# Kernel optimization log

Hardware: AMD Instinct MI355X
Metric: run time of the kernel (lower is better)

Reference implementation:

```python
import jax, jax.numpy as jnp
import numpy as np

EPS = 1e-7

def segment_softmax(logits, seg, num_segments):
    # Numerically-stable softmax over edges grouped by destination node,
    # applied independently per feature column (logits: [E, D]).
    m = jax.ops.segment_max(logits, seg, num_segments=num_segments)  # [N, D]
    e = jnp.exp(logits - m[seg])                                     # [E, D]
    s = jax.ops.segment_sum(e, seg, num_segments=num_segments)       # [N, D]
    return e / s[seg]

def setup_inputs() -> dict:
    key = jax.random.key(0)
    N, E, D_IN, D_OUT = 50000, 800000, 64, 64
    ks = jax.random.split(key, 4)
    x = jax.random.normal(ks[0], (N, D_IN), dtype=jnp.float32)
    edge_index = jax.random.randint(ks[1], (2, E), 0, N, dtype=jnp.int64)
    # nn.Linear(in_feat, out_feat) params
    W = jax.random.normal(ks[2], (D_OUT, D_IN), dtype=jnp.float32) * (1.0 / np.sqrt(D_IN))
    b = jax.random.normal(ks[3], (D_OUT,), dtype=jnp.float32) * 0.01
    beta = jnp.ones((1,), dtype=jnp.float32)  # aggr='softmax_sg' beta parameter
    return {"x": x, "W": W, "b": b, "beta": beta, "edge_index": edge_index}

def reference(x, W, b, beta, edge_index):
    N = x.shape[0]
    dst = edge_index[0]  # scatter / softmax segment ids
    src = edge_index[1]  # gather ids
    # gather + ReLU + eps
    edge_msg = jax.nn.relu(x[src]) + EPS                    # [E, D]
    # softmax_sg aggregation: softmax of beta*msg over incoming edges of each dst
    a = segment_softmax(beta * edge_msg, dst, N)            # [E, D]
    h = jax.ops.segment_sum(edge_msg * a, dst, num_segments=N)  # [N, D]
    # final Linear
    return h @ W.T + b
```

## Files before the change

kernel.cpp:

```cpp
#include <hip/hip_runtime.h>
#include <hip/hip_fp16.h>

#define EPS 1e-7f
#define EPB 4096
#define CSTRIDE 16
#define BSH 7
#define BN  128
#define CAP 64

__device__ __forceinline__ void pack_body(const float4* __restrict__ x4,
                                          short4* __restrict__ xh, int i, int nq) {
    if (i < nq) {
        float4 v = x4[i];
        short4 o;
        o.x = __half_as_short(__float2half_rn(fmaxf(v.x, 0.f) + EPS));
        o.y = __half_as_short(__float2half_rn(fmaxf(v.y, 0.f) + EPS));
        o.z = __half_as_short(__float2half_rn(fmaxf(v.z, 0.f) + EPS));
        o.w = __half_as_short(__float2half_rn(fmaxf(v.w, 0.f) + EPS));
        xh[i] = o;
    }
}

__global__ __launch_bounds__(256) void part_kernel(const float4* __restrict__ x4,
                                                   short4* __restrict__ xh, int nq,
                                                   int packBlocks,
                                                   const int* __restrict__ ei, int E,
                                                   int CAPB,
                                                   int* __restrict__ cursor,
                                                   unsigned int* __restrict__ partArr) {
    int bb = blockIdx.x;
    int tid = threadIdx.x;
    if (bb < packBlocks) {
        pack_body(x4, xh, bb * 256 + tid, nq);
        return;
    }
    __shared__ int hist[512];
    __shared__ int off[512];
    int blk = bb - packBlocks;
    hist[tid] = 0;
    hist[tid + 256] = 0;
    __syncthreads();

    int base = blk * EPB;
    int dd[16], ss[16], bk[16], rk[16];
    #pragma unroll
    for (int k = 0; k < 16; ++k) {
        int e = base + k * 256 + tid;
        bk[k] = -1;
        if (e < E) {
            dd[k] = ei[e];
            ss[k] = ei[E + e];
            bk[k] = dd[k] >> BSH;
            rk[k] = atomicAdd(&hist[bk[k]], 1);
        }
    }
    __syncthreads();
    int hv = hist[tid];
    if (hv > 0) off[tid] = atomicAdd(&cursor[tid * CSTRIDE], hv);
    int hv2 = hist[tid + 256];
    if (hv2 > 0) off[tid + 256] = atomicAdd(&cursor[(tid + 256) * CSTRIDE], hv2);
    __syncthreads();
    #pragma unroll
    for (int k = 0; k < 16; ++k) {
        if (bk[k] >= 0) {
            int idx = off[bk[k]] + rk[k];
            if (idx < CAPB)
                partArr[(size_t)bk[k] * CAPB + idx] =
                    ((unsigned int)dd[k] << 16) | (unsigned int)ss[k];
        }
    }
}

__global__ __launch_bounds__(512) void agg_kernel(const unsigned int* __restrict__ partArr,
                                                  const int* __restrict__ cursor,
                                                  int CAPB,
                                                  const __half* __restrict__ xh,
                                                  const float* __restrict__ beta_p,
                                                  float* __restrict__ out, int N) {
    __shared__ unsigned short sl[BN * CAP];
    __shared__ int hist[BN];
    int tid = threadIdx.x;
    int bkt = blockIdx.x;
    if (tid < BN) hist[tid] = 0;
    __syncthreads();

    int cnt = cursor[bkt * CSTRIDE];
    if (cnt > CAPB) cnt = CAPB;
    const unsigned int* pa = partArr + (size_t)bkt * CAPB;
    for (int i = tid; i < cnt; i += 512) {
        unsigned int u = pa[i];
        int ln = (u >> 16) & (BN - 1);
        int r = atomicAdd(&hist[ln], 1);
        if (r < CAP) sl[ln * CAP + r] = (unsigned short)(u & 0xFFFF);
    }
    __syncthreads();

    float beta = beta_p[0];
    int lane = tid & 63;
    int w = tid >> 6;

    for (int t = 0; t < BN / 8; ++t) {
        int ln = w * (BN / 8) + t;
        int n = (bkt << BSH) + ln;
        if (n >= N) continue;
        int dg = hist[ln];
        if (dg > CAP) dg = CAP;
        int myid = (lane < dg) ? (int)sl[ln * CAP + lane] : 0;

        float s = 0.0f, tt = 0.0f;
        #define ACCV(wv, j) { float m = __half2float(wv); float e = __expf(beta * m); \
                              e = (i + (j) < dg) ? e : 0.0f; \
                              s += e; tt = fmaf(m, e, tt); }
        for (int i = 0; i < dg; i += 8) {
            const __half* q0 = xh + (__builtin_amdgcn_readlane(myid, i + 0) << 6);
            const __half* q1 = xh + (__builtin_amdgcn_readlane(myid, i + 1) << 6);
            const __half* q2 = xh + (__builtin_amdgcn_readlane(myid, i + 2) << 6);
            const __half* q3 = xh + (__builtin_amdgcn_readlane(myid, i + 3) << 6);
            const __half* q4 = xh + (__builtin_amdgcn_readlane(myid, i + 4) << 6);
            const __half* q5 = xh + (__builtin_amdgcn_readlane(myid, i + 5) << 6);
            const __half* q6 = xh + (__builtin_amdgcn_readlane(myid, i + 6) << 6);
            const __half* q7 = xh + (__builtin_amdgcn_readlane(myid, i + 7) << 6);
            __half w0 = q0[lane], w1 = q1[lane], w2 = q2[lane], w3 = q3[lane];
            __half w4 = q4[lane], w5 = q5[lane], w6 = q6[lane], w7 = q7[lane];
            ACCV(w0, 0) ACCV(w1, 1) ACCV(w2, 2) ACCV(w3, 3)
            ACCV(w4, 4) ACCV(w5, 5) ACCV(w6, 6) ACCV(w7, 7)
        }
        #undef ACCV
        out[(size_t)n * 64 + lane] = (dg > 0) ? (tt / s) : 0.0f;
    }
}

#define GS 65
__global__ __launch_bounds__(256) void gemm_kernel(float* __restrict__ out,
                                                   const float* __restrict__ W,
                                                   const float* __restrict__ b,
                                                   int N) {
    __shared__ float hl[64 * GS];
    __shared__ float Wt[64 * GS];
    int tid  = threadIdx.x;
    int row0 = blockIdx.x * 64;

    #pragma unroll
    for (int kk = 0; kk < 4; ++kk) {
        int i4 = kk * 256 + tid;
        int rj = i4 >> 4;
        int d0 = (i4 & 15) * 4;
        float4 wv = *(const float4*)(W + (size_t)i4 * 4);
        Wt[(d0 + 0) * GS + rj] = wv.x;
        Wt[(d0 + 1) * GS + rj] = wv.y;
        Wt[(d0 + 2) * GS + rj] = wv.z;
        Wt[(d0 + 3) * GS + rj] = wv.w;
        float4 hv = (row0 + rj < N)
                  ? *(const float4*)(out + (size_t)row0 * 64 + (size_t)i4 * 4)
                  : make_float4(0.f, 0.f, 0.f, 0.f);
        hl[rj * GS + d0 + 0] = hv.x;
        hl[rj * GS + d0 + 1] = hv.y;
        hl[rj * GS + d0 + 2] = hv.z;
        hl[rj * GS + d0 + 3] = hv.w;
    }
    __syncthreads();

    int c4 = tid & 15;
    int r4 = tid >> 4;
    float4 bv = *(const float4*)(b + c4 * 4);
    float acc[4][4];
    #pragma unroll
    for (int ri = 0; ri < 4; ++ri) {
        acc[ri][0] = bv.x; acc[ri][1] = bv.y; acc[ri][2] = bv.z; acc[ri][3] = bv.w;
    }
    #pragma unroll 8
    for (int d = 0; d < 64; ++d) {
        float h0 = hl[(r4 * 4 + 0) * GS + d];
        float h1 = hl[(r4 * 4 + 1) * GS + d];
        float h2 = hl[(r4 * 4 + 2) * GS + d];
        float h3 = hl[(r4 * 4 + 3) * GS + d];
        float w0 = Wt[d * GS + c4 * 4 + 0];
        float w1 = Wt[d * GS + c4 * 4 + 1];
        float w2 = Wt[d * GS + c4 * 4 + 2];
        float w3 = Wt[d * GS + c4 * 4 + 3];
        acc[0][0] = fmaf(h0, w0, acc[0][0]); acc[0][1] = fmaf(h0, w1, acc[0][1]);
        acc[0][2] = fmaf(h0, w2, acc[0][2]); acc[0][3] = fmaf(h0, w3, acc[0][3]);
        acc[1][0] = fmaf(h1, w0, acc[1][0]); acc[1][1] = fmaf(h1, w1, acc[1][1]);
        acc[1][2] = fmaf(h1, w2, acc[1][2]); acc[1][3] = fmaf(h1, w3, acc[1][3]);
        acc[2][0] = fmaf(h2, w0, acc[2][0]); acc[2][1] = fmaf(h2, w1, acc[2][1]);
        acc[2][2] = fmaf(h2, w2, acc[2][2]); acc[2][3] = fmaf(h2, w3, acc[2][3]);
        acc[3][0] = fmaf(h3, w0, acc[3][0]); acc[3][1] = fmaf(h3, w1, acc[3][1]);
        acc[3][2] = fmaf(h3, w2, acc[3][2]); acc[3][3] = fmaf(h3, w3, acc[3][3]);
    }
    #pragma unroll
    for (int ri = 0; ri < 4; ++ri) {
        int row = row0 + r4 * 4 + ri;
        if (row < N) {
            *(float4*)(out + (size_t)row * 64 + c4 * 4) =
                make_float4(acc[ri][0], acc[ri][1], acc[ri][2], acc[ri][3]);
        }
    }
}

extern "C" void kernel_launch(void* const* d_in, const int* in_sizes, int n_in,
                              void* d_out, int out_size, void* d_ws, size_t ws_size,
                              hipStream_t stream) {
    const float* x      = (const float*)d_in[0];
    const float* W      = (const float*)d_in[1];
    const float* b      = (const float*)d_in[2];
    const float* beta_p = (const float*)d_in[3];
    const int*   ei     = (const int*)d_in[4];

    int NT = in_sizes[0];
    int N  = NT / 64;
    int E  = in_sizes[4] / 2;

    int NBK = (N + BN - 1) >> BSH;
    int pblocks = (NT / 4 + 255) / 256;
    int eblocks = (E + EPB - 1) / EPB;

    size_t curB   = (size_t)512 * CSTRIDE * 4;
    size_t fixedB = curB + (size_t)NT * 2;
    int CAPB = (int)(((size_t)2 * E / NBK + 4095) & ~(size_t)4095);
    if (ws_size < fixedB + (size_t)NBK * CAPB * 4) {
        size_t avail = (ws_size > fixedB) ? (ws_size - fixedB) : 0;
        int fitc = (int)(avail / ((size_t)NBK * 4));
        CAPB = (fitc / 64) * 64;
        if (CAPB <= 0) return;
    }

    char* p = (char*)d_ws;
    int* cursor           = (int*)p;                      p += curB;
    unsigned int* partArr = (unsigned int*)p;             p += (size_t)NBK * CAPB * 4;
    __half* xh            = (__half*)p;

    hipMemsetAsync(cursor, 0, curB, stream);

    part_kernel<<<pblocks + eblocks, 256, 0, stream>>>(
        (const float4*)x, (short4*)xh, NT / 4, pblocks, ei, E, CAPB, cursor, partArr);

    agg_kernel<<<NBK, 512, 0, stream>>>(partArr, cursor, CAPB, xh, beta_p,
                                        (float*)d_out, N);

    gemm_kernel<<<(N + 63) / 64, 256, 0, stream>>>((float*)d_out, W, b, N);
}
```

Measured before the change: 149.0 us.

## Split aggregation into 4-node blocks with XCD-aware block remapping

The aggregation kernel used to give each 512-thread block a 128-node bucket. It now launches one 256-thread block per 4 destination nodes, with one wavefront per node. Partition buckets shrink to 64 nodes, so the partition kernel's histogram grows to 1024 entries and the bucket capacity rounding is tightened. Block indices are remapped so that consecutive node groups land on the same XCD, which is meant to keep the shared bucket's edge list in that chiplet's L2. The aim is far more blocks and better load balance across CUs, at the cost of each block rescanning its whole 64-node bucket, about 16 times redundant edge-list reads.

Result: faster. 144.1 us (-3.3%).

```diff
diff --git a/kernel.cpp b/kernel.cpp
--- a/kernel.cpp
+++ b/kernel.cpp
@@ -4,9 +4,8 @@
 #define EPS 1e-7f
 #define EPB 4096
 #define CSTRIDE 16
-#define BSH 7
-#define BN  128
-#define CAP 64
+#define BSH 6
+#define BN  64
 
 __device__ __forceinline__ void pack_body(const float4* __restrict__ x4,
                                           short4* __restrict__ xh, int i, int nq) {
@@ -34,11 +33,11 @@
         pack_body(x4, xh, bb * 256 + tid, nq);
         return;
     }
-    __shared__ int hist[512];
-    __shared__ int off[512];
+    __shared__ int hist[1024];
+    __shared__ int off[1024];
     int blk = bb - packBlocks;
-    hist[tid] = 0;
-    hist[tid + 256] = 0;
+    #pragma unroll
+    for (int j = 0; j < 4; ++j) hist[tid + j * 256] = 0;
     __syncthreads();
 
     int base = blk * EPB;
@@ -55,10 +54,12 @@
         }
     }
     __syncthreads();
-    int hv = hist[tid];
-    if (hv > 0) off[tid] = atomicAdd(&cursor[tid * CSTRIDE], hv);
-    int hv2 = hist[tid + 256];
-    if (hv2 > 0) off[tid + 256] = atomicAdd(&cursor[(tid + 256) * CSTRIDE], hv2);
+    #pragma unroll
+    for (int j = 0; j < 4; ++j) {
+        int s = tid + j * 256;
+        int hv = hist[s];
+        if (hv > 0) off[s] = atomicAdd(&cursor[s * CSTRIDE], hv);
+    }
     __syncthreads();
     #pragma unroll
     for (int k = 0; k < 16; ++k) {
@@ -71,63 +72,66 @@
     }
 }
 
-__global__ __launch_bounds__(512) void agg_kernel(const unsigned int* __restrict__ partArr,
-                                                  const int* __restrict__ cursor,
-                                                  int CAPB,
-                                                  const __half* __restrict__ xh,
-                                                  const float* __restrict__ beta_p,
-                                                  float* __restrict__ out, int N) {
-    __shared__ unsigned short sl[BN * CAP];
-    __shared__ int hist[BN];
+__global__ __launch_bounds__(256) void main_kernel(const unsigned int* __restrict__ partArr,
+                                                   const int* __restrict__ cursor,
+                                                   int CAPB,
+                                                   const __half* __restrict__ xh,
+                                                   const float* __restrict__ beta_p,
+                                                   float* __restrict__ out, int N,
+                                                   int q, int r) {
+    __shared__ unsigned short sl[4 * 64];
+    __shared__ int hist[4];
     int tid = threadIdx.x;
-    int bkt = blockIdx.x;
-    if (tid < BN) hist[tid] = 0;
-    __syncthreads();
-
+    int b = blockIdx.x;
+    int x = b & 7;
+    int m = (x < r ? x * (q + 1) : r * (q + 1) + (x - r) * q) + (b >> 3);
+    int n0 = m << 2;
+    if (tid < 4) hist[tid] = 0;
+    __syncthreads();
+
+    int bkt = m >> 4;
     int cnt = cursor[bkt * CSTRIDE];
     if (cnt > CAPB) cnt = CAPB;
     const unsigned int* pa = partArr + (size_t)bkt * CAPB;
-    for (int i = tid; i < cnt; i += 512) {
+    for (int i = tid; i < cnt; i += 256) {
         unsigned int u = pa[i];
-        int ln = (u >> 16) & (BN - 1);
-        int r = atomicAdd(&hist[ln], 1);
-        if (r < CAP) sl[ln * CAP + r] = (unsigned short)(u & 0xFFFF);
-    }
-    __syncthreads();
-
-    float beta = beta_p[0];
+        int rel = (int)(u >> 16) - n0;
+        if ((unsigned)rel < 4u) {
+            int rr = atomicAdd(&hist[rel], 1);
+            if (rr < 64) sl[(rel << 6) + rr] = (unsigned short)(u & 0xFFFF);
+        }
+    }
+    __syncthreads();
+
     int lane = tid & 63;
     int w = tid >> 6;
-
-    for (int t = 0; t < BN / 8; ++t) {
-        int ln = w * (BN / 8) + t;
-        int n = (bkt << BSH) + ln;
-        if (n >= N) continue;
-        int dg = hist[ln];
-        if (dg > CAP) dg = CAP;
-        int myid = (lane < dg) ? (int)sl[ln * CAP + lane] : 0;
-
-        float s = 0.0f, tt = 0.0f;
-        #define ACCV(wv, j) { float m = __half2float(wv); float e = __expf(beta * m); \
-                              e = (i + (j) < dg) ? e : 0.0f; \
-                              s += e; tt = fmaf(m, e, tt); }
-        for (int i = 0; i < dg; i += 8) {
-            const __half* q0 = xh + (__builtin_amdgcn_readlane(myid, i + 0) << 6);
-            const __half* q1 = xh + (__builtin_amdgcn_readlane(myid, i + 1) << 6);
-            const __half* q2 = xh + (__builtin_amdgcn_readlane(myid, i + 2) << 6);
-            const __half* q3 = xh + (__builtin_amdgcn_readlane(myid, i + 3) << 6);
-            const __half* q4 = xh + (__builtin_amdgcn_readlane(myid, i + 4) << 6);
-            const __half* q5 = xh + (__builtin_amdgcn_readlane(myid, i + 5) << 6);
-            const __half* q6 = xh + (__builtin_amdgcn_readlane(myid, i + 6) << 6);
-            const __half* q7 = xh + (__builtin_amdgcn_readlane(myid, i + 7) << 6);
-            __half w0 = q0[lane], w1 = q1[lane], w2 = q2[lane], w3 = q3[lane];
-            __half w4 = q4[lane], w5 = q5[lane], w6 = q6[lane], w7 = q7[lane];
-            ACCV(w0, 0) ACCV(w1, 1) ACCV(w2, 2) ACCV(w3, 3)
-            ACCV(w4, 4) ACCV(w5, 5) ACCV(w6, 6) ACCV(w7, 7)
-        }
-        #undef ACCV
-        out[(size_t)n * 64 + lane] = (dg > 0) ? (tt / s) : 0.0f;
-    }
+    int n = n0 + w;
+    if (n >= N) return;
+    float beta = beta_p[0];
+    int dg = hist[w];
+    if (dg > 64) dg = 64;
+    int myid = (lane < dg) ? (int)sl[(w << 6) + lane] : 0;
+
+    float s = 0.0f, t = 0.0f;
+    #define ACCV(wv, j) { float mm = __half2float(wv); float e = __expf(beta * mm); \
+                          e = (i + (j) < dg) ? e : 0.0f; \
+                          s += e; t = fmaf(mm, e, t); }
+    for (int i = 0; i < dg; i += 8) {
+        const __half* q0 = xh + (__builtin_amdgcn_readlane(myid, i + 0) << 6);
+        const __half* q1 = xh + (__builtin_amdgcn_readlane(myid, i + 1) << 6);
+        const __half* q2 = xh + (__builtin_amdgcn_readlane(myid, i + 2) << 6);
+        const __half* q3 = xh + (__builtin_amdgcn_readlane(myid, i + 3) << 6);
+        const __half* q4 = xh + (__builtin_amdgcn_readlane(myid, i + 4) << 6);
+        const __half* q5 = xh + (__builtin_amdgcn_readlane(myid, i + 5) << 6);
+        const __half* q6 = xh + (__builtin_amdgcn_readlane(myid, i + 6) << 6);
+        const __half* q7 = xh + (__builtin_amdgcn_readlane(myid, i + 7) << 6);
+        __half w0 = q0[lane], w1 = q1[lane], w2 = q2[lane], w3 = q3[lane];
+        __half w4 = q4[lane], w5 = q5[lane], w6 = q6[lane], w7 = q7[lane];
+        ACCV(w0, 0) ACCV(w1, 1) ACCV(w2, 2) ACCV(w3, 3)
+        ACCV(w4, 4) ACCV(w5, 5) ACCV(w6, 6) ACCV(w7, 7)
+    }
+    #undef ACCV
+    out[(size_t)n * 64 + lane] = (dg > 0) ? (t / s) : 0.0f;
 }
 
 #define GS 65
@@ -213,10 +217,12 @@
     int NBK = (N + BN - 1) >> BSH;
     int pblocks = (NT / 4 + 255) / 256;
     int eblocks = (E + EPB - 1) / EPB;
-
-    size_t curB   = (size_t)512 * CSTRIDE * 4;
+    int nblk = (N + 3) / 4;
+    int q = nblk / 8, r = nblk % 8;
+
+    size_t curB   = (size_t)NBK * CSTRIDE * 4;
     size_t fixedB = curB + (size_t)NT * 2;
-    int CAPB = (int)(((size_t)2 * E / NBK + 4095) & ~(size_t)4095);
+    int CAPB = (int)(((size_t)2 * E / NBK + 255) & ~(size_t)255);
     if (ws_size < fixedB + (size_t)NBK * CAPB * 4) {
         size_t avail = (ws_size > fixedB) ? (ws_size - fixedB) : 0;
         int fitc = (int)(avail / ((size_t)NBK * 4));
@@ -234,8 +240,8 @@
     part_kernel<<<pblocks + eblocks, 256, 0, stream>>>(
         (const float4*)x, (short4*)xh, NT / 4, pblocks, ei, E, CAPB, cursor, partArr);
 
-    agg_kernel<<<NBK, 512, 0, stream>>>(partArr, cursor, CAPB, xh, beta_p,
-                                        (float*)d_out, N);
+    main_kernel<<<nblk, 256, 0, stream>>>(partArr, cursor, CAPB, xh, beta_p,
+                                          (float*)d_out, N, q, r);
 
     gemm_kernel<<<(N + 63) / 64, 256, 0, stream>>>((float*)d_out, W, b, N);
 }
```
